# Kernel tuning notes

Measured on AMD Instinct MI355X. Metric: run time of the kernel, lower is better.

The kernel has to match this reference:

```python
import jax, jax.numpy as jnp
import numpy as np

H = 2          # h_dim (hard-coded in PPIModel)
L = 4          # n_hid rgcn layers
R = 16         # num_rels
B = 8          # num_bases
N = 1_000_000  # num_nodes
E = 16_000_000 # num_edges


def setup_inputs() -> dict:
    key = jax.random.key(0)
    ks = jax.random.split(key, 10)
    features = jax.random.normal(ks[0], (N * H,), dtype=jnp.float32)
    edge_src = jax.random.randint(ks[1], (E,), 0, N)
    edge_dst = jax.random.randint(ks[2], (E,), 0, N)
    edge_type = jax.random.randint(ks[3], (E,), 0, R)
    norm = jax.random.uniform(ks[4], (E, 1), dtype=jnp.float32)
    # Basis-decomposition params per layer: W_r = sum_b comp[r,b] * V[b]
    V = jax.random.normal(ks[5], (L, B, H, H), dtype=jnp.float32) / np.sqrt(H)
    comp = jax.random.normal(ks[6], (L, R, B), dtype=jnp.float32) / np.sqrt(B)
    bias = jnp.zeros((L, H), dtype=jnp.float32)  # DGL RelGraphConv h_bias (default bias=True)
    w_mlp = jax.random.normal(ks[7], (1, N * H), dtype=jnp.float32) / np.sqrt(N * H)
    b_mlp = jnp.zeros((1,), dtype=jnp.float32)
    return dict(features=features, norm=norm, V=V, comp=comp, bias=bias,
                w_mlp=w_mlp, b_mlp=b_mlp,
                edge_src=edge_src, edge_dst=edge_dst, edge_type=edge_type)


def reference(features, norm, V, comp, bias, w_mlp, b_mlp, edge_src, edge_dst, edge_type):
    x = features.reshape(-1, H)          # [N, 2]
    skip = x
    for i in range(L):
        # relation weights from bases: [R, H, H]
        W = jnp.einsum('rb,bio->rio', comp[i], V[i])
        # message per edge: gather src feats, apply relation weight, scale by norm
        msg = jnp.einsum('ei,eio->eo', x[edge_src], W[edge_type]) * norm  # [E, 2]
        # scatter-sum to destination nodes
        h = jax.ops.segment_sum(msg, edge_dst, num_segments=N) + bias[i]  # [N, 2]
        if i < L - 1:
            h = jax.nn.relu(h)
        x = h
        if i % 2 == 1:
            x = x + skip
            skip = x
    flat = x.reshape(1, N * H)           # [1, 2N]
    logit = flat @ w_mlp.T + b_mlp       # [1, 1]
    return jax.nn.sigmoid(logit)
```

## Files before the change

### kernel.cpp

```cpp
#include <hip/hip_runtime.h>
#include <hip/hip_bf16.h>
#include <hip/hip_fp16.h>

#define HD 2
#define LAYERS 4
#define RELS 16
#define BASES 8

#define BSH   10
#define NB    1024
#define NBINS (1 << BSH)
#define SBLK  512
#define TPB   256
#define CAP   18176
#define OVFCAP 40960
#define LCAP  6144

static const int SUBSORT_LDS_BYTES = CAP * 8 + NBINS * 4 + 64;


__global__ void prep_kernel(const float* __restrict__ V, const float* __restrict__ comp,
                            float* __restrict__ W, float* __restrict__ acc,
                            unsigned* __restrict__ ovfctr) {
    int idx = threadIdx.x;
    if (idx < LAYERS * RELS * 4) {
        int l  = idx >> 6;
        int r  = (idx >> 2) & (RELS - 1);
        int io = idx & 3;
        float s = 0.f;
        for (int b = 0; b < BASES; ++b)
            s += comp[(l * RELS + r) * BASES + b] * V[(l * BASES + b) * 4 + io];
        W[idx] = s;
    }
    if (idx == 0) { *acc = 0.f; *ovfctr = 0u; }
}

__global__ void finalize_kernel(const float* __restrict__ acc,
                                const float* __restrict__ b_mlp,
                                float* __restrict__ out) {
    float v = *acc + b_mlp[0];
    out[0] = 1.f / (1.f + expf(-v));
}

__global__ __launch_bounds__(TPB) void f2h_kernel(const float2* __restrict__ f,
                                                  __half2* __restrict__ h, int N) {
    int i = blockIdx.x * TPB + threadIdx.x;
    int stride = gridDim.x * TPB;
    for (; i < N; i += stride)
        h[i] = __float22half2_rn(f[i]);
}


__global__ __launch_bounds__(TPB) void hist_kernel(const int* __restrict__ dst,
                                                   unsigned* __restrict__ blockhist,
                                                   int E, int per) {
    __shared__ unsigned hist[NB];
    for (int i = threadIdx.x; i < NB; i += TPB) hist[i] = 0u;
    __syncthreads();
    int blk = blockIdx.x;
    int e0 = blk * per;
    int e1 = min(e0 + per, E);
    const int4* dst4 = (const int4*)dst;
    int g0 = e0 >> 2, g1 = e1 >> 2;
    for (int g = g0 + threadIdx.x; g < g1; g += TPB) {
        int4 d = dst4[g];
        atomicAdd(&hist[((unsigned)d.x) >> BSH], 1u);
        atomicAdd(&hist[((unsigned)d.y) >> BSH], 1u);
        atomicAdd(&hist[((unsigned)d.z) >> BSH], 1u);
        atomicAdd(&hist[((unsigned)d.w) >> BSH], 1u);
    }
    for (int e = (g1 << 2) + threadIdx.x; e < e1; e += TPB)
        atomicAdd(&hist[((unsigned)dst[e]) >> BSH], 1u);
    __syncthreads();
    for (int i = threadIdx.x; i < NB; i += TPB)
        blockhist[(size_t)blk * NB + i] = hist[i];
}

__global__ __launch_bounds__(TPB) void colscan_kernel(unsigned* __restrict__ blockhist,
                                                      unsigned* __restrict__ totals) {
    int bucket = blockIdx.x;
    int t = threadIdx.x;
    unsigned v0 = blockhist[(size_t)(2 * t)     * NB + bucket];
    unsigned v1 = blockhist[(size_t)(2 * t + 1) * NB + bucket];
    unsigned run = v0 + v1;
    __shared__ unsigned s[TPB];
    s[t] = run;
    __syncthreads();
    for (int off = 1; off < TPB; off <<= 1) {
        unsigned x = (t >= off) ? s[t - off] : 0u;
        __syncthreads();
        s[t] += x;
        __syncthreads();
    }
    unsigned base = s[t] - run;
    blockhist[(size_t)(2 * t)     * NB + bucket] = base;
    blockhist[(size_t)(2 * t + 1) * NB + bucket] = base + v0;
    if (t == TPB - 1) totals[bucket] = s[TPB - 1];
}

__global__ __launch_bounds__(TPB) void scan_kernel(const unsigned* __restrict__ totals,
                                                   unsigned* __restrict__ base) {
    int t = threadIdx.x;
    unsigned v[4]; unsigned run = 0;
#pragma unroll
    for (int k = 0; k < 4; ++k) { v[k] = run; run += totals[4 * t + k]; }
    __shared__ unsigned s[TPB];
    s[t] = run;
    __syncthreads();
    for (int off = 1; off < TPB; off <<= 1) {
        unsigned x = (t >= off) ? s[t - off] : 0u;
        __syncthreads();
        s[t] += x;
        __syncthreads();
    }
    unsigned b0 = s[t] - run;
#pragma unroll
    for (int k = 0; k < 4; ++k) base[4 * t + k] = b0 + v[k];
    if (t == TPB - 1) base[NB] = s[TPB - 1];
}

__global__ __launch_bounds__(TPB) void scatter_kernel(const int* __restrict__ src,
                                                      const int* __restrict__ dst,
                                                      const int* __restrict__ typ,
                                                      const float* __restrict__ norm,
                                                      const unsigned* __restrict__ blockhist,
                                                      const unsigned* __restrict__ base,
                                                      uint2* __restrict__ packed,
                                                      int E, int per) {
    __shared__ unsigned cnt[NB];
    int blk = blockIdx.x;
    for (int i = threadIdx.x; i < NB; i += TPB)
        cnt[i] = blockhist[(size_t)blk * NB + i] + base[i];
    __syncthreads();
    int e0 = blk * per;
    int e1 = min(e0 + per, E);
    const int4*   src4 = (const int4*)src;
    const int4*   dst4 = (const int4*)dst;
    const int4*   typ4 = (const int4*)typ;
    const float4* nrm4 = (const float4*)norm;
    int g0 = e0 >> 2, g1 = e1 >> 2;

#define PUT(SS, DD, TT, NN)                                                       \
    {                                                                             \
        unsigned _d = (unsigned)(DD);                                             \
        unsigned _bucket = _d >> BSH;                                             \
        unsigned _pos = atomicAdd(&cnt[_bucket], 1u);                             \
        unsigned _w1 = (_d & ((1u << BSH) - 1u)) | (((unsigned)(TT)) << 12) |     \
                       ((unsigned)__half_as_ushort(__float2half_rn(NN)) << 16);   \
        packed[_pos] = make_uint2((unsigned)(SS), _w1);                           \
    }

    for (int g = g0 + threadIdx.x; g < g1; g += TPB) {
        int4 s = src4[g];
        int4 d = dst4[g];
        int4 t = typ4[g];
        float4 nm = nrm4[g];
        PUT(s.x, d.x, t.x, nm.x)
        PUT(s.y, d.y, t.y, nm.y)
        PUT(s.z, d.z, t.z, nm.z)
        PUT(s.w, d.w, t.w, nm.w)
    }
    for (int e = (g1 << 2) + threadIdx.x; e < e1; e += TPB)
        PUT(src[e], dst[e], typ[e], norm[e])
#undef PUT
}

__global__ __launch_bounds__(TPB) void subsort_kernel(
    unsigned long long* __restrict__ packed8,
    const unsigned* __restrict__ base,
    unsigned* __restrict__ off,
    unsigned long long* __restrict__ ovfbuf,
    unsigned* __restrict__ ovfctr,
    int N, int E)
{
    extern __shared__ unsigned long long smem[];
    unsigned long long* stage = smem;
    unsigned* hist  = (unsigned*)(smem + CAP);
    unsigned* wpart = hist + NBINS;

    int b = blockIdx.x;
    int t = threadIdx.x;
    unsigned e0 = base[b], e1 = base[b + 1];
    unsigned len = e1 - e0;

    __shared__ unsigned long long* gs;
    if (len > CAP) {
        if (t == 0) {
            unsigned slot = atomicAdd(ovfctr, 1u) % 6u;
            gs = ovfbuf + (size_t)slot * OVFCAP;
        }
        __syncthreads();
        stage = gs;
    }

    for (int i = t; i < NBINS; i += TPB) hist[i] = 0u;
    __syncthreads();

    for (unsigned i = t; i < len; i += TPB) {
        unsigned long long q = packed8[e0 + i];
        stage[i] = q;
        atomicAdd(&hist[(unsigned)(q >> 32) & (NBINS - 1u)], 1u);
    }
    __syncthreads();

    unsigned loc[4]; unsigned run = 0;
#pragma unroll
    for (int k = 0; k < 4; ++k) { loc[k] = run; run += hist[t * 4 + k]; }

    unsigned lane = t & 63, wv = t >> 6;
    unsigned v = run;
    for (int o = 1; o < 64; o <<= 1) {
        unsigned u = __shfl_up(v, o, 64);
        if (lane >= (unsigned)o) v += u;
    }
    if (lane == 63) wpart[wv] = v;
    __syncthreads();
    unsigned wbase = 0;
    for (int w = 0; w < (int)(TPB / 64); ++w) if ((unsigned)w < wv) wbase += wpart[w];
    unsigned excl = wbase + v - run;

    unsigned nodeBase = (unsigned)b << BSH;
#pragma unroll
    for (int k = 0; k < 4; ++k) {
        unsigned bin = (unsigned)(t * 4 + k);
        unsigned pos = e0 + excl + loc[k];
        hist[bin] = pos;
        unsigned node = nodeBase + bin;
        if (node < (unsigned)N) off[node] = pos;
    }
    if (b == 0 && t == 0) off[N] = (unsigned)E;
    __syncthreads();

    for (unsigned i = t; i < len; i += TPB) {
        unsigned long long q = stage[i];
        unsigned bin = (unsigned)(q >> 32) & (NBINS - 1u);
        unsigned pos = atomicAdd(&hist[bin], 1u);
        packed8[pos] = q;
    }
}

__global__ __launch_bounds__(TPB) void csr_edge_kernel(
    const unsigned long long* __restrict__ rec8,
    const unsigned* __restrict__ off,
    const __half2* __restrict__ xh,
    const float* __restrict__ Wl,
    const float* __restrict__ bias2,
    const __half2* __restrict__ skiph,
    __half2* __restrict__ outh,
    const float2* __restrict__ w2,
    float* __restrict__ acc,
    int N, int do_relu)
{
    __shared__ float sW[64];
    __shared__ float wred[TPB / 64];
    __shared__ unsigned slo[LCAP];
    __shared__ unsigned shi[LCAP];
    int t = threadIdx.x;
    if (t < 64) sW[t] = Wl[t];

    int d0   = blockIdx.x * TPB;
    int dmax = min(d0 + TPB, N);
    unsigned e0 = off[d0];
    unsigned eE = off[dmax];
    unsigned len = eE - e0;
    bool useLds = (len <= (unsigned)LCAP);

    if (useLds) {
        for (unsigned i = t; i < len; i += TPB) {
            unsigned long long q = __builtin_nontemporal_load(&rec8[e0 + i]);
            unsigned sw = i ^ ((i >> 4) & 15u);
            slo[sw] = (unsigned)q;
            shi[sw] = (unsigned)(q >> 32);
        }
    }
    __syncthreads();

    int d = d0 + t;
    float r0 = 0.f, r1 = 0.f;
    if (d < N) {
        unsigned ea = off[d], eb = off[d + 1];
        if (useLds) {
            for (unsigned e = ea - e0; e < eb - e0; ++e) {
                unsigned sw = e ^ ((e >> 4) & 15u);
                unsigned s = slo[sw];
                unsigned m = shi[sw];
                __half2 hv = xh[s];
                float x0 = __low2float(hv), x1 = __high2float(hv);
                int wb = (int)((m >> 12) & 15u) << 2;
                float nm = __half2float(__ushort_as_half((unsigned short)(m >> 16)));
                r0 += (x0 * sW[wb + 0] + x1 * sW[wb + 2]) * nm;
                r1 += (x0 * sW[wb + 1] + x1 * sW[wb + 3]) * nm;
            }
        } else {
            for (unsigned e = ea; e < eb; ++e) {
                unsigned long long q = __builtin_nontemporal_load(&rec8[e]);
                unsigned m = (unsigned)(q >> 32);
                __half2 hv = xh[(unsigned)q];
                float x0 = __low2float(hv), x1 = __high2float(hv);
                int wb = (int)((m >> 12) & 15u) << 2;
                float nm = __half2float(__ushort_as_half((unsigned short)(m >> 16)));
                r0 += (x0 * sW[wb + 0] + x1 * sW[wb + 2]) * nm;
                r1 += (x0 * sW[wb + 1] + x1 * sW[wb + 3]) * nm;
            }
        }
        r0 += bias2[0]; r1 += bias2[1];
        if (do_relu) { r0 = fmaxf(r0, 0.f); r1 = fmaxf(r1, 0.f); }
        if (skiph) { __half2 sv = skiph[d]; r0 += __low2float(sv); r1 += __high2float(sv); }
        if (outh) outh[d] = __float22half2_rn(make_float2(r0, r1));
    }
    if (w2) {
        float part = 0.f;
        if (d < N) { float2 wv = w2[d]; part = r0 * wv.x + r1 * wv.y; }
        for (int o = 32; o > 0; o >>= 1) part += __shfl_down(part, o, 64);
        if ((t & 63) == 0) wred[t >> 6] = part;
        __syncthreads();
        if (t == 0) {
            float s = 0.f;
            for (int w = 0; w < (int)(TPB / 64); ++w) s += wred[w];
            atomicAdd(acc, s);
        }
    }
}


__global__ void zero_kernel(float4* __restrict__ p, int n4) {
    int i = blockIdx.x * blockDim.x + threadIdx.x;
    int stride = gridDim.x * blockDim.x;
    for (; i < n4; i += stride) p[i] = make_float4(0.f, 0.f, 0.f, 0.f);
}

__global__ __launch_bounds__(256) void edge_kernel(
    const float* __restrict__ x, const int* __restrict__ src,
    const int* __restrict__ dst, const int* __restrict__ typ,
    const float* __restrict__ norm, const float* __restrict__ Wl,
    float* __restrict__ h, int E)
{
    __shared__ float sW[64];
    if (threadIdx.x < 64) sW[threadIdx.x] = Wl[threadIdx.x];
    __syncthreads();
    const float2* __restrict__ x2 = (const float2*)x;
    int tid = blockIdx.x * blockDim.x + threadIdx.x;
    int stride = gridDim.x * blockDim.x;
    for (int e = tid; e < E; e += stride) {
        int s = src[e], d = dst[e], t = typ[e];
        float nm = norm[e];
        float2 xv = x2[s];
        int wb = t << 2;
        float m0 = (xv.x * sW[wb + 0] + xv.y * sW[wb + 2]) * nm;
        float m1 = (xv.x * sW[wb + 1] + xv.y * sW[wb + 3]) * nm;
        atomicAdd(&h[2 * (size_t)d],     m0);
        atomicAdd(&h[2 * (size_t)d + 1], m1);
    }
}

__global__ void node_kernel(const float* __restrict__ h, const float* __restrict__ bias_l,
                            const float* __restrict__ skip, float* __restrict__ xout,
                            int N, int do_relu)
{
    float b0 = bias_l[0], b1 = bias_l[1];
    const float2* __restrict__ h2 = (const float2*)h;
    const float2* __restrict__ s2 = (const float2*)skip;
    float2* __restrict__ o2 = (float2*)xout;
    int i = blockIdx.x * blockDim.x + threadIdx.x;
    int stride = gridDim.x * blockDim.x;
    for (; i < N; i += stride) {
        float2 v = h2[i];
        v.x += b0; v.y += b1;
        if (do_relu) { v.x = fmaxf(v.x, 0.f); v.y = fmaxf(v.y, 0.f); }
        if (skip) { float2 sv = s2[i]; v.x += sv.x; v.y += sv.y; }
        o2[i] = v;
    }
}

__global__ __launch_bounds__(256) void dot_kernel(const float* __restrict__ a,
                                                  const float* __restrict__ b,
                                                  float* __restrict__ acc, int n)
{
    int i = blockIdx.x * blockDim.x + threadIdx.x;
    int stride = gridDim.x * blockDim.x;
    float s = 0.f;
    int n4 = n >> 2;
    const float4* __restrict__ a4 = (const float4*)a;
    const float4* __restrict__ b4 = (const float4*)b;
    for (int g = i; g < n4; g += stride) {
        float4 av = a4[g], bv = b4[g];
        s += av.x * bv.x + av.y * bv.y + av.z * bv.z + av.w * bv.w;
    }
    for (int e = (n4 << 2) + i; e < n; e += stride) s += a[e] * b[e];
    for (int off = 32; off > 0; off >>= 1) s += __shfl_down(s, off, 64);
    __shared__ float wsum[4];
    int lane = threadIdx.x & 63, wv = threadIdx.x >> 6;
    if (lane == 0) wsum[wv] = s;
    __syncthreads();
    if (threadIdx.x == 0) atomicAdd(acc, wsum[0] + wsum[1] + wsum[2] + wsum[3]);
}


static inline size_t align256(size_t x) { return (x + 255) & ~(size_t)255; }

extern "C" void kernel_launch(void* const* d_in, const int* in_sizes, int n_in,
                              void* d_out, int out_size, void* d_ws, size_t ws_size,
                              hipStream_t stream) {
    const float* features = (const float*)d_in[0];
    const float* norm     = (const float*)d_in[1];
    const float* V        = (const float*)d_in[2];
    const float* comp     = (const float*)d_in[3];
    const float* bias     = (const float*)d_in[4];
    const float* w_mlp    = (const float*)d_in[5];
    const float* b_mlp    = (const float*)d_in[6];
    const int*   esrc     = (const int*)d_in[7];
    const int*   edst     = (const int*)d_in[8];
    const int*   etyp     = (const int*)d_in[9];

    int NH = in_sizes[0];
    int N  = NH / 2;
    int E  = in_sizes[7];

    char* ws = (char*)d_ws;
    size_t oW    = 0;
    size_t oAcc  = align256(oW + 1024);
    size_t oOvf  = align256(oAcc + 4);
    size_t oBase = align256(oOvf + 4);
    size_t oTot  = align256(oBase + (size_t)(NB + 1) * 4);
    size_t oFH   = align256(oTot + (size_t)NB * 4);
    size_t oAH   = align256(oFH + (size_t)N * 4);
    size_t oBH   = align256(oAH + (size_t)N * 4);
    size_t oCH   = align256(oBH + (size_t)N * 4);
    size_t oOff  = align256(oCH + (size_t)N * 4);
    size_t oHist = align256(oOff + (size_t)(N + 1) * 4);
    size_t oPack = align256(oHist + (size_t)SBLK * NB * 4);
    size_t REQ   = oPack + (size_t)E * 8;

    float* A = (float*)(ws + oFH);
    float* B = (float*)(ws + oBH);
    float* C = (float*)(ws + oPack);

    float* W      = (float*)(ws + oW);
    float* acc    = (float*)(ws + oAcc);
    unsigned* ovfctr = (unsigned*)(ws + oOvf);

    prep_kernel<<<1, 256, 0, stream>>>(V, comp, W, acc, ovfctr);

    if (ws_size >= REQ && N <= (1 << 20)) {
        __half2* FH = (__half2*)(ws + oFH);
        __half2* AH = (__half2*)(ws + oAH);
        __half2* BH = (__half2*)(ws + oBH);
        __half2* CH = (__half2*)(ws + oCH);
        unsigned* base      = (unsigned*)(ws + oBase);
        unsigned* totals    = (unsigned*)(ws + oTot);
        unsigned* offArr    = (unsigned*)(ws + oOff);
        unsigned* blockhist = (unsigned*)(ws + oHist);
        uint2*    packed    = (uint2*)(ws + oPack);
        unsigned long long* packed8 = (unsigned long long*)packed;

        int per = (((E + SBLK - 1) / SBLK) + 3) & ~3;
        int nbkt = (N + NBINS - 1) >> BSH;

        static bool attr_done = false;
        if (!attr_done) {
            (void)hipFuncSetAttribute((const void*)subsort_kernel,
                                      hipFuncAttributeMaxDynamicSharedMemorySize,
                                      SUBSORT_LDS_BYTES);
            attr_done = true;
        }

        int cb = min((N + TPB - 1) / TPB, 2048);
        f2h_kernel    <<<cb,   TPB, 0, stream>>>((const float2*)features, FH, N);
        hist_kernel   <<<SBLK, TPB, 0, stream>>>(edst, blockhist, E, per);
        colscan_kernel<<<NB,   TPB, 0, stream>>>(blockhist, totals);
        scan_kernel   <<<1,    TPB, 0, stream>>>(totals, base);
        scatter_kernel<<<SBLK, TPB, 0, stream>>>(esrc, edst, etyp, norm,
                                                 blockhist, base, packed, E, per);
        subsort_kernel<<<nbkt, TPB, SUBSORT_LDS_BYTES, stream>>>(
            packed8, base, offArr, (unsigned long long*)blockhist, ovfctr, N, E);

        int ngrid = (N + TPB - 1) / TPB;
        const float2* w2 = (const float2*)w_mlp;

        csr_edge_kernel<<<ngrid, TPB, 0, stream>>>(packed8, offArr, FH, W + 0,
            bias + 0, nullptr, AH, nullptr, acc, N, 1);
        csr_edge_kernel<<<ngrid, TPB, 0, stream>>>(packed8, offArr, AH, W + 64,
            bias + 2, FH, BH, nullptr, acc, N, 1);
        csr_edge_kernel<<<ngrid, TPB, 0, stream>>>(packed8, offArr, BH, W + 128,
            bias + 4, nullptr, CH, nullptr, acc, N, 1);
        csr_edge_kernel<<<ngrid, TPB, 0, stream>>>(packed8, offArr, CH, W + 192,
            bias + 6, BH, nullptr, w2, acc, N, 0);
    } else {
        int zb = (NH / 4 + 255) / 256;
        int eb = (E / 4 + 255) / 256;
        int nb = (N + 255) / 256;
        int db = (NH / 4 + 255) / 256;

        zero_kernel<<<zb, 256, 0, stream>>>((float4*)A, NH / 4);
        edge_kernel<<<eb, 256, 0, stream>>>(features, esrc, edst, etyp, norm, W + 0, A, E);
        node_kernel<<<nb, 256, 0, stream>>>(A, bias + 0, nullptr, A, N, 1);

        zero_kernel<<<zb, 256, 0, stream>>>((float4*)B, NH / 4);
        edge_kernel<<<eb, 256, 0, stream>>>(A, esrc, edst, etyp, norm, W + 64, B, E);
        node_kernel<<<nb, 256, 0, stream>>>(B, bias + 2, features, B, N, 1);

        zero_kernel<<<zb, 256, 0, stream>>>((float4*)C, NH / 4);
        edge_kernel<<<eb, 256, 0, stream>>>(B, esrc, edst, etyp, norm, W + 128, C, E);
        node_kernel<<<nb, 256, 0, stream>>>(C, bias + 4, nullptr, C, N, 1);

        zero_kernel<<<zb, 256, 0, stream>>>((float4*)A, NH / 4);
        edge_kernel<<<eb, 256, 0, stream>>>(C, esrc, edst, etyp, norm, W + 192, A, E);
        node_kernel<<<nb, 256, 0, stream>>>(A, bias + 6, B, A, N, 0);

        dot_kernel<<<db, 256, 0, stream>>>(A, w_mlp, acc, NH);
    }

    finalize_kernel<<<1, 1, 0, stream>>>(acc, b_mlp, (float*)d_out);
}
```

Before: 1.203 ms.

## Stage scatter chunks in LDS by bucket before coalesced global writes; unroll CSR gather

The scatter kernel now processes edges in 8192-edge chunks. For each chunk it builds a local bucket histogram, does a block-wide scan, and sorts records into LDS by destination bucket. It then writes them out so that consecutive threads store to contiguous runs in the global packed array, replacing scattered 8-byte stores. The cost is extra passes over dst, a binary search per output element, and a large dynamic LDS allocation that lowers occupancy. Separately, the CSR edge-accumulation loop over LDS-staged records is unrolled by four so more feature gathers are in flight at once.

```diff
diff --git a/kernel.cpp b/kernel.cpp
--- a/kernel.cpp
+++ b/kernel.cpp
@@ -15,8 +15,10 @@
 #define CAP   18176
 #define OVFCAP 40960
 #define LCAP  6144
+#define SCHUNK 8192
 
 static const int SUBSORT_LDS_BYTES = CAP * 8 + NBINS * 4 + 64;
+static const int SCATTER_LDS_BYTES = SCHUNK * 8 + NB * 4 * 3 + 64;
 
 
 __global__ void prep_kernel(const float* __restrict__ V, const float* __restrict__ comp,
@@ -127,42 +129,79 @@
                                                       const unsigned* __restrict__ base,
                                                       uint2* __restrict__ packed,
                                                       int E, int per) {
-    __shared__ unsigned cnt[NB];
+    extern __shared__ char scmem[];
+    uint2*    staged   = (uint2*)scmem;
+    unsigned* cnt      = (unsigned*)(scmem + SCHUNK * 8);
+    unsigned* hist     = cnt + NB;
+    unsigned* binStart = hist + NB;
+    unsigned* wpart    = binStart + NB + 1;
+
     int blk = blockIdx.x;
-    for (int i = threadIdx.x; i < NB; i += TPB)
+    int t = threadIdx.x;
+    for (int i = t; i < NB; i += TPB)
         cnt[i] = blockhist[(size_t)blk * NB + i] + base[i];
-    __syncthreads();
+
     int e0 = blk * per;
     int e1 = min(e0 + per, E);
-    const int4*   src4 = (const int4*)src;
-    const int4*   dst4 = (const int4*)dst;
-    const int4*   typ4 = (const int4*)typ;
-    const float4* nrm4 = (const float4*)norm;
-    int g0 = e0 >> 2, g1 = e1 >> 2;
-
-#define PUT(SS, DD, TT, NN)                                                       \
-    {                                                                             \
-        unsigned _d = (unsigned)(DD);                                             \
-        unsigned _bucket = _d >> BSH;                                             \
-        unsigned _pos = atomicAdd(&cnt[_bucket], 1u);                             \
-        unsigned _w1 = (_d & ((1u << BSH) - 1u)) | (((unsigned)(TT)) << 12) |     \
-                       ((unsigned)__half_as_ushort(__float2half_rn(NN)) << 16);   \
-        packed[_pos] = make_uint2((unsigned)(SS), _w1);                           \
-    }
-
-    for (int g = g0 + threadIdx.x; g < g1; g += TPB) {
-        int4 s = src4[g];
-        int4 d = dst4[g];
-        int4 t = typ4[g];
-        float4 nm = nrm4[g];
-        PUT(s.x, d.x, t.x, nm.x)
-        PUT(s.y, d.y, t.y, nm.y)
-        PUT(s.z, d.z, t.z, nm.z)
-        PUT(s.w, d.w, t.w, nm.w)
-    }
-    for (int e = (g1 << 2) + threadIdx.x; e < e1; e += TPB)
-        PUT(src[e], dst[e], typ[e], norm[e])
-#undef PUT
+
+    for (int cs = e0; cs < e1; cs += SCHUNK) {
+        int clen = min(SCHUNK, e1 - cs);
+
+        for (int i = t; i < NB; i += TPB) hist[i] = 0u;
+        __syncthreads();
+        for (int i = t; i < clen; i += TPB)
+            atomicAdd(&hist[((unsigned)dst[cs + i]) >> BSH], 1u);
+        __syncthreads();
+
+        unsigned loc[4]; unsigned run = 0;
+#pragma unroll
+        for (int k = 0; k < 4; ++k) { loc[k] = run; run += hist[t * 4 + k]; }
+        unsigned lane = t & 63, wv = t >> 6;
+        unsigned v = run;
+        for (int o = 1; o < 64; o <<= 1) {
+            unsigned u = __shfl_up(v, o, 64);
+            if (lane >= (unsigned)o) v += u;
+        }
+        if (lane == 63) wpart[wv] = v;
+        __syncthreads();
+        unsigned wbase = 0;
+        for (int w = 0; w < (int)(TPB / 64); ++w) if ((unsigned)w < wv) wbase += wpart[w];
+        unsigned excl = wbase + v - run;
+#pragma unroll
+        for (int k = 0; k < 4; ++k) {
+            unsigned bin = (unsigned)(t * 4 + k);
+            unsigned p = excl + loc[k];
+            binStart[bin] = p;
+            hist[bin] = p;
+        }
+        if (t == TPB - 1) binStart[NB] = excl + run;
+        __syncthreads();
+
+        for (int i = t; i < clen; i += TPB) {
+            int e = cs + i;
+            unsigned d = (unsigned)dst[e];
+            unsigned b = d >> BSH;
+            unsigned pos = atomicAdd(&hist[b], 1u);
+            unsigned w1 = (d & (NBINS - 1u)) | (((unsigned)typ[e]) << 12) |
+                          ((unsigned)__half_as_ushort(__float2half_rn(norm[e])) << 16);
+            staged[pos] = make_uint2((unsigned)src[e], w1);
+        }
+        __syncthreads();
+
+        for (int i = t; i < clen; i += TPB) {
+            unsigned lo = 0, hi = NB;
+#pragma unroll
+            for (int s = 0; s < 10; ++s) {
+                unsigned mid = (lo + hi) >> 1;
+                if (binStart[mid] <= (unsigned)i) lo = mid; else hi = mid;
+            }
+            packed[cnt[lo] + ((unsigned)i - binStart[lo])] = staged[i];
+        }
+        __syncthreads();
+
+        for (int b = t; b < NB; b += TPB) cnt[b] += binStart[b + 1] - binStart[b];
+        __syncthreads();
+    }
 }
 
 __global__ __launch_bounds__(TPB) void subsort_kernel(
@@ -275,32 +314,48 @@
     }
     __syncthreads();
 
+#define ACC(HV, M)                                                                 \
+    {                                                                              \
+        float x0 = __low2float(HV), x1 = __high2float(HV);                         \
+        int wb = (int)(((M) >> 12) & 15u) << 2;                                    \
+        float nm = __half2float(__ushort_as_half((unsigned short)((M) >> 16)));    \
+        r0 += (x0 * sW[wb + 0] + x1 * sW[wb + 2]) * nm;                            \
+        r1 += (x0 * sW[wb + 1] + x1 * sW[wb + 3]) * nm;                            \
+    }
+
     int d = d0 + t;
     float r0 = 0.f, r1 = 0.f;
     if (d < N) {
         unsigned ea = off[d], eb = off[d + 1];
         if (useLds) {
-            for (unsigned e = ea - e0; e < eb - e0; ++e) {
-                unsigned sw = e ^ ((e >> 4) & 15u);
-                unsigned s = slo[sw];
-                unsigned m = shi[sw];
+            unsigned i = ea - e0, ib = eb - e0;
+            for (; i + 4 <= ib; i += 4) {
+                unsigned sw0 = (i)     ^ (((i)     >> 4) & 15u);
+                unsigned sw1 = (i + 1) ^ (((i + 1) >> 4) & 15u);
+                unsigned sw2 = (i + 2) ^ (((i + 2) >> 4) & 15u);
+                unsigned sw3 = (i + 3) ^ (((i + 3) >> 4) & 15u);
+                unsigned s0 = slo[sw0], m0 = shi[sw0];
+                unsigned s1 = slo[sw1], m1 = shi[sw1];
+                unsigned s2 = slo[sw2], m2 = shi[sw2];
+                unsigned s3 = slo[sw3], m3 = shi[sw3];
+                __half2 h0 = xh[s0];
+                __half2 h1 = xh[s1];
+                __half2 h2 = xh[s2];
+                __half2 h3 = xh[s3];
+                ACC(h0, m0) ACC(h1, m1) ACC(h2, m2) ACC(h3, m3)
+            }
+            for (; i < ib; ++i) {
+                unsigned sw = i ^ ((i >> 4) & 15u);
+                unsigned s = slo[sw], m = shi[sw];
                 __half2 hv = xh[s];
-                float x0 = __low2float(hv), x1 = __high2float(hv);
-                int wb = (int)((m >> 12) & 15u) << 2;
-                float nm = __half2float(__ushort_as_half((unsigned short)(m >> 16)));
-                r0 += (x0 * sW[wb + 0] + x1 * sW[wb + 2]) * nm;
-                r1 += (x0 * sW[wb + 1] + x1 * sW[wb + 3]) * nm;
+                ACC(hv, m)
             }
         } else {
             for (unsigned e = ea; e < eb; ++e) {
                 unsigned long long q = __builtin_nontemporal_load(&rec8[e]);
                 unsigned m = (unsigned)(q >> 32);
                 __half2 hv = xh[(unsigned)q];
-                float x0 = __low2float(hv), x1 = __high2float(hv);
-                int wb = (int)((m >> 12) & 15u) << 2;
-                float nm = __half2float(__ushort_as_half((unsigned short)(m >> 16)));
-                r0 += (x0 * sW[wb + 0] + x1 * sW[wb + 2]) * nm;
-                r1 += (x0 * sW[wb + 1] + x1 * sW[wb + 3]) * nm;
+                ACC(hv, m)
             }
         }
         r0 += bias2[0]; r1 += bias2[1];
@@ -308,6 +363,7 @@
         if (skiph) { __half2 sv = skiph[d]; r0 += __low2float(sv); r1 += __high2float(sv); }
         if (outh) outh[d] = __float22half2_rn(make_float2(r0, r1));
     }
+#undef ACC
     if (w2) {
         float part = 0.f;
         if (d < N) { float2 wv = w2[d]; part = r0 * wv.x + r1 * wv.y; }
@@ -461,6 +517,9 @@
             (void)hipFuncSetAttribute((const void*)subsort_kernel,
                                       hipFuncAttributeMaxDynamicSharedMemorySize,
                                       SUBSORT_LDS_BYTES);
+            (void)hipFuncSetAttribute((const void*)scatter_kernel,
+                                      hipFuncAttributeMaxDynamicSharedMemorySize,
+                                      SCATTER_LDS_BYTES);
             attr_done = true;
         }
 
@@ -469,8 +528,8 @@
         hist_kernel   <<<SBLK, TPB, 0, stream>>>(edst, blockhist, E, per);
         colscan_kernel<<<NB,   TPB, 0, stream>>>(blockhist, totals);
         scan_kernel   <<<1,    TPB, 0, stream>>>(totals, base);
-        scatter_kernel<<<SBLK, TPB, 0, stream>>>(esrc, edst, etyp, norm,
-                                                 blockhist, base, packed, E, per);
+        scatter_kernel<<<SBLK, TPB, SCATTER_LDS_BYTES, stream>>>(
+            esrc, edst, etyp, norm, blockhist, base, packed, E, per);
         subsort_kernel<<<nbkt, TPB, SUBSORT_LDS_BYTES, stream>>>(
             packed8, base, offArr, (unsigned long long*)blockhist, ovfctr, N, E);
 
```

Result: slower. 1.240 ms (+3.1%).
